# Performance work log

Measured on AMD Instinct MI355X. Metric: run time of the kernel, lower is better.

The kernel has to match this reference:

```python
import jax, jax.numpy as jnp
import numpy as np

N_NODES = 50000
D = 256
N_EDGES = 262144
N_LAYER = 3
EPS = 1e-5


def setup_inputs() -> dict:
    key = jax.random.key(0)
    ks = jax.random.split(key, 8)
    x = jax.random.normal(ks[0], (N_NODES, D), dtype=jnp.float32)
    jg_edge_index = jax.random.randint(ks[1], (2, N_EDGES), 0, N_NODES, dtype=jnp.int64)
    ln_w = jnp.ones((D,), dtype=jnp.float32)
    # torch Linear weight is [out, in]; stack per-layer weights [L, D, D]
    Ws = jax.random.normal(ks[2], (N_LAYER, D, D), dtype=jnp.float32) * (1.0 / np.sqrt(D))
    gammas = jnp.ones((N_LAYER, D), dtype=jnp.float32)
    betas = jnp.zeros((N_LAYER, D), dtype=jnp.float32)
    W_out = jax.random.normal(ks[3], (1, D), dtype=jnp.float32) * (1.0 / np.sqrt(D))
    return {"x": x, "jg_edge_index": jg_edge_index, "ln_w": ln_w,
            "Ws": Ws, "gammas": gammas, "betas": betas, "W_out": W_out}


def reference(x, jg_edge_index, ln_w, Ws, gammas, betas, W_out):
    src, dst = jg_edge_index[0], jg_edge_index[1]
    # edge features: gather + add -> [E, D]
    h = x[src, :] + x[dst, :]
    # LayerNorm over feature dim, weight only (bias=False), eps=1e-5
    mu = jnp.mean(h, axis=-1, keepdims=True)
    var = jnp.mean(jnp.square(h - mu), axis=-1, keepdims=True)
    h = (h - mu) * jax.lax.rsqrt(var + EPS) * ln_w
    # projection blocks: Linear (no bias) -> BatchNorm1d (training stats) -> ReLU
    for i in range(N_LAYER):
        h = h @ Ws[i].T  # [E, D]
        bmu = jnp.mean(h, axis=0)                      # batch mean over edges
        bvar = jnp.mean(jnp.square(h - bmu), axis=0)   # biased batch var
        h = (h - bmu) * jax.lax.rsqrt(bvar + EPS) * gammas[i] + betas[i]
        h = jax.nn.relu(h)
    logits = (h @ W_out.T).squeeze(-1)  # [E]
    return logits
```

## Files before the change

kernel.cpp:

```cpp
#include <hip/hip_runtime.h>
#include <hip/hip_bf16.h>

#define NEDGE 262144
#define DIM 256
#define NNODE 50000
#define NLAYER 3
#define EPSV 1e-5f

#define GBM 512
#define RC 64
#define NCH (GBM / RC)
#define GEMM_GRID (NEDGE / GBM)

typedef __attribute__((ext_vector_type(8))) short bf16x8_t;
typedef __attribute__((ext_vector_type(4))) float f32x4_t;

__device__ __forceinline__ float bf2f(short s) {
  unsigned u = ((unsigned)(unsigned short)s) << 16;
  return __builtin_bit_cast(float, u);
}
__device__ __forceinline__ short f2bf(float f) {
  __hip_bfloat16 h = __float2bfloat16(f);
  return __builtin_bit_cast(short, h);
}

extern "C" __global__ void __launch_bounds__(256)
k_cvt(const float* __restrict__ src, short* __restrict__ dst, int n) {
  int i = blockIdx.x * 256 + threadIdx.x;
  if (i < n) dst[i] = f2bf(src[i]);
}

extern "C" __global__ void __launch_bounds__(256)
k_cvt_x(const float* __restrict__ src, short* __restrict__ dst, int n8) {
  int i = blockIdx.x * 256 + threadIdx.x;
  if (i >= n8) return;
  const float4 a = *(const float4*)(src + (size_t)i * 8);
  const float4 b = *(const float4*)(src + (size_t)i * 8 + 4);
  bf16x8_t o;
  o[0] = f2bf(a.x); o[1] = f2bf(a.y); o[2] = f2bf(a.z); o[3] = f2bf(a.w);
  o[4] = f2bf(b.x); o[5] = f2bf(b.y); o[6] = f2bf(b.z); o[7] = f2bf(b.w);
  *(bf16x8_t*)(dst + (size_t)i * 8) = o;
}

extern "C" __global__ void __launch_bounds__(512)
k_gemm1f(const short* __restrict__ xb, const int* __restrict__ ei,
         const float* __restrict__ lnw, const short* __restrict__ W,
         short* __restrict__ C, float* __restrict__ psum, float* __restrict__ psq) {
  __shared__ short As[2][RC * DIM];
  __shared__ int sIdx[GBM], dIdx[GBM];
  const int tid = threadIdx.x;
  const int w = tid >> 6;
  const int lane = tid & 63;
  const int rl = lane & 15;
  const int kh = lane >> 4;
  const int row0 = blockIdx.x * GBM;
  const int colbase = w * 32;
  const int cst = tid & 31;

  sIdx[tid] = ei[row0 + tid];
  dIdx[tid] = ei[NEDGE + row0 + tid];

  bf16x8_t wf[2][8];
#pragma unroll
  for (int n = 0; n < 2; ++n)
#pragma unroll
    for (int ks = 0; ks < 8; ++ks)
      wf[n][ks] = *(const bf16x8_t*)(W + (size_t)(colbase + n * 16 + rl) * DIM + ks * 32 + kh * 8);

  float lw[8];
#pragma unroll
  for (int j = 0; j < 8; ++j) lw[j] = lnw[cst * 8 + j];

  float st_s0 = 0.f, st_s1 = 0.f, st_q0 = 0.f, st_q1 = 0.f;

  bf16x8_t rsA[4], rdA[4], rsB[4], rdB[4];

  auto ldgA = [&](int t) {
#pragma unroll
    for (int i = 0; i < 4; ++i) {
      const int r = (tid >> 5) + 16 * i;
      const int s = sIdx[t * RC + r];
      const int d = dIdx[t * RC + r];
      rsA[i] = *(const bf16x8_t*)(xb + (size_t)s * DIM + cst * 8);
      rdA[i] = *(const bf16x8_t*)(xb + (size_t)d * DIM + cst * 8);
    }
  };
  auto ldgB = [&](int t) {
#pragma unroll
    for (int i = 0; i < 4; ++i) {
      const int r = (tid >> 5) + 16 * i;
      const int s = sIdx[t * RC + r];
      const int d = dIdx[t * RC + r];
      rsB[i] = *(const bf16x8_t*)(xb + (size_t)s * DIM + cst * 8);
      rdB[i] = *(const bf16x8_t*)(xb + (size_t)d * DIM + cst * 8);
    }
  };

  auto lnwr = [&](int b, bf16x8_t* rs, bf16x8_t* rd) {
#pragma unroll
    for (int i = 0; i < 4; ++i) {
      const int r = (tid >> 5) + 16 * i;
      float v[8];
#pragma unroll
      for (int j = 0; j < 8; ++j) v[j] = bf2f(rs[i][j]) + bf2f(rd[i][j]);
      float s = 0.f, ss = 0.f;
#pragma unroll
      for (int j = 0; j < 8; ++j) { s += v[j]; ss = fmaf(v[j], v[j], ss); }
#pragma unroll
      for (int off = 16; off >= 1; off >>= 1) {
        s += __shfl_xor(s, off);
        ss += __shfl_xor(ss, off);
      }
      const float mu = s * (1.0f / DIM);
      const float var = ss * (1.0f / DIM) - mu * mu;
      const float sc = rsqrtf(var + EPSV);
      bf16x8_t o;
#pragma unroll
      for (int j = 0; j < 8; ++j) o[j] = f2bf((v[j] - mu) * sc * lw[j]);
      *(bf16x8_t*)(&As[b][r * DIM + ((cst ^ (r & 7)) << 3)]) = o;
    }
  };

  auto compute = [&](int t, int b) {
    const f32x4_t zero = {0.f, 0.f, 0.f, 0.f};
    f32x4_t acc[4][2];
#pragma unroll
    for (int m = 0; m < 4; ++m) { acc[m][0] = zero; acc[m][1] = zero; }
    const short* base = As[b];
#pragma unroll
    for (int ks = 0; ks < 8; ++ks) {
      bf16x8_t af[4];
#pragma unroll
      for (int m = 0; m < 4; ++m) {
        const int row = m * 16 + rl;
        const int c = ks * 4 + kh;
        af[m] = *(const bf16x8_t*)(base + row * DIM + ((c ^ (row & 7)) << 3));
      }
#pragma unroll
      for (int m = 0; m < 4; ++m) {
        acc[m][0] = __builtin_amdgcn_mfma_f32_16x16x32_bf16(af[m], wf[0][ks], acc[m][0], 0, 0, 0);
        acc[m][1] = __builtin_amdgcn_mfma_f32_16x16x32_bf16(af[m], wf[1][ks], acc[m][1], 0, 0, 0);
      }
    }
    const int rquad = kh << 2;
#pragma unroll
    for (int n = 0; n < 2; ++n) {
      const int col = colbase + n * 16 + rl;
      float s = 0.f, q = 0.f;
#pragma unroll
      for (int m = 0; m < 4; ++m) {
        const size_t rb = (size_t)(row0 + t * RC + m * 16 + rquad) * DIM + col;
#pragma unroll
        for (int r = 0; r < 4; ++r) {
          const float f = acc[m][n][r];
          C[rb + (size_t)r * DIM] = f2bf(f);
          s += f;
          q = fmaf(f, f, q);
        }
      }
      if (n == 0) { st_s0 += s; st_q0 += q; }
      else        { st_s1 += s; st_q1 += q; }
    }
  };

  __syncthreads();
  ldgA(0);
  ldgB(1);
  lnwr(0, rsA, rdA);
  __syncthreads();
  for (int t = 0; t < NCH; t += 2) {
    if (t + 2 < NCH) ldgA(t + 2);
    compute(t, 0);
    lnwr(1, rsB, rdB);
    __syncthreads();
    if (t + 3 < NCH) ldgB(t + 3);
    compute(t + 1, 1);
    if (t + 2 < NCH) lnwr(0, rsA, rdA);
    __syncthreads();
  }

  {
    float s = st_s0, q = st_q0;
    s += __shfl_xor(s, 16); s += __shfl_xor(s, 32);
    q += __shfl_xor(q, 16); q += __shfl_xor(q, 32);
    if (lane < 16) {
      psum[(size_t)blockIdx.x * DIM + colbase + rl] = s;
      psq [(size_t)blockIdx.x * DIM + colbase + rl] = q;
    }
  }
  {
    float s = st_s1, q = st_q1;
    s += __shfl_xor(s, 16); s += __shfl_xor(s, 32);
    q += __shfl_xor(q, 16); q += __shfl_xor(q, 32);
    if (lane < 16) {
      psum[(size_t)blockIdx.x * DIM + colbase + 16 + rl] = s;
      psq [(size_t)blockIdx.x * DIM + colbase + 16 + rl] = q;
    }
  }
}

extern "C" __global__ void __launch_bounds__(512, 2)
k_gemm_bn(const short* __restrict__ A, const short* __restrict__ W,
          short* __restrict__ C, float* __restrict__ psum, float* __restrict__ psq,
          const float* __restrict__ bsc, const float* __restrict__ bsh) {
  __shared__ short As[2][RC * DIM];
  const int tid = threadIdx.x;
  const int w = tid >> 6;
  const int lane = tid & 63;
  const int rl = lane & 15;
  const int kh = lane >> 4;
  const int row0 = blockIdx.x * GBM;
  const int colbase = w * 32;

  bf16x8_t wf[2][8];
#pragma unroll
  for (int n = 0; n < 2; ++n)
#pragma unroll
    for (int ks = 0; ks < 8; ++ks)
      wf[n][ks] = *(const bf16x8_t*)(W + (size_t)(colbase + n * 16 + rl) * DIM + ks * 32 + kh * 8);

  const int cst = tid & 31;
  float sc0[8], sh0[8];
#pragma unroll
  for (int j = 0; j < 8; ++j) {
    sc0[j] = bsc[cst * 8 + j];
    sh0[j] = bsh[cst * 8 + j];
  }

  float st_s0 = 0.f, st_s1 = 0.f, st_q0 = 0.f, st_q1 = 0.f;

  auto ldreg = [&](int t, bf16x8_t* r) {
#pragma unroll
    for (int i = 0; i < 4; ++i) {
      const int row = (tid + i * 512) >> 5;
      r[i] = *(const bf16x8_t*)(A + (size_t)(row0 + t * RC + row) * DIM + cst * 8);
    }
  };
  auto xform_write = [&](int b, bf16x8_t* r) {
#pragma unroll
    for (int i = 0; i < 4; ++i) {
      const int row = (tid + i * 512) >> 5;
      bf16x8_t v = r[i];
      bf16x8_t o;
#pragma unroll
      for (int j = 0; j < 8; ++j)
        o[j] = f2bf(fmaxf(fmaf(bf2f(v[j]), sc0[j], sh0[j]), 0.0f));
      *(bf16x8_t*)(&As[b][row * DIM + ((cst ^ (row & 7)) << 3)]) = o;
    }
  };

  auto compute = [&](int t, int b) {
    const f32x4_t zero = {0.f, 0.f, 0.f, 0.f};
    f32x4_t acc[4][2];
#pragma unroll
    for (int m = 0; m < 4; ++m) { acc[m][0] = zero; acc[m][1] = zero; }
    const short* base = As[b];
#pragma unroll
    for (int ks = 0; ks < 8; ++ks) {
      bf16x8_t af[4];
#pragma unroll
      for (int m = 0; m < 4; ++m) {
        const int row = m * 16 + rl;
        const int c = ks * 4 + kh;
        af[m] = *(const bf16x8_t*)(base + row * DIM + ((c ^ (row & 7)) << 3));
      }
#pragma unroll
      for (int m = 0; m < 4; ++m) {
        acc[m][0] = __builtin_amdgcn_mfma_f32_16x16x32_bf16(af[m], wf[0][ks], acc[m][0], 0, 0, 0);
        acc[m][1] = __builtin_amdgcn_mfma_f32_16x16x32_bf16(af[m], wf[1][ks], acc[m][1], 0, 0, 0);
      }
    }
    const int rquad = kh << 2;
#pragma unroll
    for (int n = 0; n < 2; ++n) {
      const int col = colbase + n * 16 + rl;
      float s = 0.f, q = 0.f;
#pragma unroll
      for (int m = 0; m < 4; ++m) {
        const size_t rb = (size_t)(row0 + t * RC + m * 16 + rquad) * DIM + col;
#pragma unroll
        for (int r = 0; r < 4; ++r) {
          const float f = acc[m][n][r];
          C[rb + (size_t)r * DIM] = f2bf(f);
          s += f;
          q = fmaf(f, f, q);
        }
      }
      if (n == 0) { st_s0 += s; st_q0 += q; }
      else        { st_s1 += s; st_q1 += q; }
    }
  };

  bf16x8_t ra[4], rb[4];
  ldreg(0, ra);
  xform_write(0, ra);
  ldreg(1, rb);
  __syncthreads();
  for (int t = 0; t < NCH; ++t) {
    if (t + 2 < NCH) ldreg(t + 2, ra);
    compute(t, t & 1);
    if (t + 1 < NCH) xform_write((t + 1) & 1, rb);
    __syncthreads();
#pragma unroll
    for (int i = 0; i < 4; ++i) { bf16x8_t tmp = ra[i]; ra[i] = rb[i]; rb[i] = tmp; }
  }

  {
    float s = st_s0, q = st_q0;
    s += __shfl_xor(s, 16); s += __shfl_xor(s, 32);
    q += __shfl_xor(q, 16); q += __shfl_xor(q, 32);
    if (lane < 16) {
      psum[(size_t)blockIdx.x * DIM + colbase + rl] = s;
      psq [(size_t)blockIdx.x * DIM + colbase + rl] = q;
    }
  }
  {
    float s = st_s1, q = st_q1;
    s += __shfl_xor(s, 16); s += __shfl_xor(s, 32);
    q += __shfl_xor(q, 16); q += __shfl_xor(q, 32);
    if (lane < 16) {
      psum[(size_t)blockIdx.x * DIM + colbase + 16 + rl] = s;
      psq [(size_t)blockIdx.x * DIM + colbase + 16 + rl] = q;
    }
  }
}

extern "C" __global__ void __launch_bounds__(64)
k_stats(const float* __restrict__ psum, const float* __restrict__ psq,
        const float* __restrict__ gamma, const float* __restrict__ beta,
        float* __restrict__ sc, float* __restrict__ sh, int nblk) {
  const int c = blockIdx.x;
  const int lane = threadIdx.x;
  float s = 0.0f, q = 0.0f;
  for (int b = lane; b < nblk; b += 64) {
    s += psum[(size_t)b * DIM + c];
    q += psq[(size_t)b * DIM + c];
  }
#pragma unroll
  for (int off = 32; off >= 1; off >>= 1) {
    s += __shfl_xor(s, off);
    q += __shfl_xor(q, off);
  }
  if (lane == 0) {
    const float inv = 1.0f / NEDGE;
    const float mu = s * inv;
    const float var = q * inv - mu * mu;
    const float scale = rsqrtf(var + EPSV) * gamma[c];
    sc[c] = scale;
    sh[c] = beta[c] - mu * scale;
  }
}

extern "C" __global__ void __launch_bounds__(256)
k_head(const short* __restrict__ h3, const float* __restrict__ sc,
       const float* __restrict__ sh, const float* __restrict__ wout,
       float* __restrict__ out) {
  const int e = (blockIdx.x << 3) + (threadIdx.x >> 5);
  const int g = threadIdx.x & 31;
  const int c = g * 8;
  const bf16x8_t v = *(const bf16x8_t*)(h3 + (size_t)e * DIM + c);
  float acc = 0.f;
#pragma unroll
  for (int j = 0; j < 8; ++j)
    acc += fmaxf(fmaf(bf2f(v[j]), sc[c + j], sh[c + j]), 0.0f) * wout[c + j];
#pragma unroll
  for (int off = 16; off >= 1; off >>= 1) acc += __shfl_xor(acc, off);
  if (g == 0) out[e] = acc;
}

extern "C" void kernel_launch(void* const* d_in, const int* in_sizes, int n_in,
                              void* d_out, int out_size, void* d_ws, size_t ws_size,
                              hipStream_t stream) {
  const float* x = (const float*)d_in[0];
  const int* ei = (const int*)d_in[1];
  const float* lnw = (const float*)d_in[2];
  const float* Ws = (const float*)d_in[3];
  const float* gammas = (const float*)d_in[4];
  const float* betas = (const float*)d_in[5];
  const float* wout = (const float*)d_in[6];
  float* out = (float*)d_out;

  char* ws = (char*)d_ws;
  const size_t HBYTES = (size_t)NEDGE * DIM * 2;
  short* h = (short*)ws;
  short* Wb = (short*)(ws + HBYTES);
  char* p = ws + HBYTES + (size_t)NLAYER * DIM * DIM * 2;
  float* psum = (float*)p;
  float* psq = psum + (size_t)GEMM_GRID * DIM;
  float* bnsc = psq + (size_t)GEMM_GRID * DIM;
  float* bnsh = bnsc + NLAYER * DIM;
  short* xb = (short*)(bnsh + NLAYER * DIM);

  k_cvt<<<(NLAYER * DIM * DIM + 255) / 256, 256, 0, stream>>>(Ws, Wb, NLAYER * DIM * DIM);
  k_cvt_x<<<(NNODE * DIM / 8 + 255) / 256, 256, 0, stream>>>(x, xb, NNODE * DIM / 8);

  k_gemm1f<<<GEMM_GRID, 512, 0, stream>>>(xb, ei, lnw, Wb, h, psum, psq);
  k_stats<<<DIM, 64, 0, stream>>>(psum, psq, gammas, betas, bnsc, bnsh, GEMM_GRID);

  for (int l = 1; l < NLAYER; ++l) {
    k_gemm_bn<<<GEMM_GRID, 512, 0, stream>>>(h, Wb + (size_t)l * DIM * DIM, h,
                                             psum, psq,
                                             bnsc + (size_t)(l - 1) * DIM,
                                             bnsh + (size_t)(l - 1) * DIM);
    k_stats<<<DIM, 64, 0, stream>>>(psum, psq, gammas + (size_t)l * DIM,
                                    betas + (size_t)l * DIM,
                                    bnsc + (size_t)l * DIM, bnsh + (size_t)l * DIM,
                                    GEMM_GRID);
  }
  k_head<<<NEDGE / 8, 256, 0, stream>>>(h, bnsc + (size_t)(NLAYER - 1) * DIM,
                                        bnsh + (size_t)(NLAYER - 1) * DIM, wout, out);
}
```

Before: 259.6 us.

## Raise GEMM-BN occupancy, stage BN scale/shift in LDS, unroll pipeline by two

The BN-fused GEMM kernel now launches with a minimum of 4 blocks per CU instead of 2. To cut register use, the per-thread BN scale/shift arrays are moved into shared memory and reloaded inside each transform. The prefetch loop is unrolled by two with fixed A/B register buffers, which removes the per-iteration register swap. The first (not-shown) GEMM kernel's C stores become nontemporal so they bypass cache retention. Risks: the tighter register budget may cause spills, and the extra LDS (two 32 KB buffers per block) may keep the occupancy target from being met.

```diff
diff --git a/kernel.cpp b/kernel.cpp
--- a/kernel.cpp
+++ b/kernel.cpp
@@ -153,7 +153,7 @@
 #pragma unroll
         for (int r = 0; r < 4; ++r) {
           const float f = acc[m][n][r];
-          C[rb + (size_t)r * DIM] = f2bf(f);
+          __builtin_nontemporal_store(f2bf(f), &C[rb + (size_t)r * DIM]);
           s += f;
           q = fmaf(f, f, q);
         }
@@ -199,11 +199,12 @@
   }
 }
 
-extern "C" __global__ void __launch_bounds__(512, 2)
+extern "C" __global__ void __launch_bounds__(512, 4)
 k_gemm_bn(const short* __restrict__ A, const short* __restrict__ W,
           short* __restrict__ C, float* __restrict__ psum, float* __restrict__ psq,
           const float* __restrict__ bsc, const float* __restrict__ bsh) {
   __shared__ short As[2][RC * DIM];
+  __shared__ float bscS[DIM], bshS[DIM];
   const int tid = threadIdx.x;
   const int w = tid >> 6;
   const int lane = tid & 63;
@@ -211,6 +212,9 @@
   const int kh = lane >> 4;
   const int row0 = blockIdx.x * GBM;
   const int colbase = w * 32;
+  const int cst = tid & 31;
+
+  if (tid < DIM) { bscS[tid] = bsc[tid]; bshS[tid] = bsh[tid]; }
 
   bf16x8_t wf[2][8];
 #pragma unroll
@@ -219,24 +223,32 @@
     for (int ks = 0; ks < 8; ++ks)
       wf[n][ks] = *(const bf16x8_t*)(W + (size_t)(colbase + n * 16 + rl) * DIM + ks * 32 + kh * 8);
 
-  const int cst = tid & 31;
-  float sc0[8], sh0[8];
-#pragma unroll
-  for (int j = 0; j < 8; ++j) {
-    sc0[j] = bsc[cst * 8 + j];
-    sh0[j] = bsh[cst * 8 + j];
-  }
-
   float st_s0 = 0.f, st_s1 = 0.f, st_q0 = 0.f, st_q1 = 0.f;
 
-  auto ldreg = [&](int t, bf16x8_t* r) {
+  bf16x8_t ra[4], rb[4];
+
+  auto ldregA = [&](int t) {
 #pragma unroll
     for (int i = 0; i < 4; ++i) {
       const int row = (tid + i * 512) >> 5;
-      r[i] = *(const bf16x8_t*)(A + (size_t)(row0 + t * RC + row) * DIM + cst * 8);
-    }
-  };
-  auto xform_write = [&](int b, bf16x8_t* r) {
+      ra[i] = *(const bf16x8_t*)(A + (size_t)(row0 + t * RC + row) * DIM + cst * 8);
+    }
+  };
+  auto ldregB = [&](int t) {
+#pragma unroll
+    for (int i = 0; i < 4; ++i) {
+      const int row = (tid + i * 512) >> 5;
+      rb[i] = *(const bf16x8_t*)(A + (size_t)(row0 + t * RC + row) * DIM + cst * 8);
+    }
+  };
+  auto xform = [&](int b, bf16x8_t* r) {
+    float cs[8], ch[8];
+    const float4 c0 = *(const float4*)&bscS[cst * 8];
+    const float4 c1 = *(const float4*)&bscS[cst * 8 + 4];
+    const float4 h0 = *(const float4*)&bshS[cst * 8];
+    const float4 h1 = *(const float4*)&bshS[cst * 8 + 4];
+    cs[0]=c0.x; cs[1]=c0.y; cs[2]=c0.z; cs[3]=c0.w; cs[4]=c1.x; cs[5]=c1.y; cs[6]=c1.z; cs[7]=c1.w;
+    ch[0]=h0.x; ch[1]=h0.y; ch[2]=h0.z; ch[3]=h0.w; ch[4]=h1.x; ch[5]=h1.y; ch[6]=h1.z; ch[7]=h1.w;
 #pragma unroll
     for (int i = 0; i < 4; ++i) {
       const int row = (tid + i * 512) >> 5;
@@ -244,7 +256,7 @@
       bf16x8_t o;
 #pragma unroll
       for (int j = 0; j < 8; ++j)
-        o[j] = f2bf(fmaxf(fmaf(bf2f(v[j]), sc0[j], sh0[j]), 0.0f));
+        o[j] = f2bf(fmaxf(fmaf(bf2f(v[j]), cs[j], ch[j]), 0.0f));
       *(bf16x8_t*)(&As[b][row * DIM + ((cst ^ (row & 7)) << 3)]) = o;
     }
   };
@@ -277,11 +289,11 @@
       float s = 0.f, q = 0.f;
 #pragma unroll
       for (int m = 0; m < 4; ++m) {
-        const size_t rb = (size_t)(row0 + t * RC + m * 16 + rquad) * DIM + col;
+        const size_t rb2 = (size_t)(row0 + t * RC + m * 16 + rquad) * DIM + col;
 #pragma unroll
         for (int r = 0; r < 4; ++r) {
           const float f = acc[m][n][r];
-          C[rb + (size_t)r * DIM] = f2bf(f);
+          C[rb2 + (size_t)r * DIM] = f2bf(f);
           s += f;
           q = fmaf(f, f, q);
         }
@@ -291,18 +303,20 @@
     }
   };
 
-  bf16x8_t ra[4], rb[4];
-  ldreg(0, ra);
-  xform_write(0, ra);
-  ldreg(1, rb);
   __syncthreads();
-  for (int t = 0; t < NCH; ++t) {
-    if (t + 2 < NCH) ldreg(t + 2, ra);
-    compute(t, t & 1);
-    if (t + 1 < NCH) xform_write((t + 1) & 1, rb);
+  ldregA(0);
+  ldregB(1);
+  xform(0, ra);
+  __syncthreads();
+  for (int t = 0; t < NCH; t += 2) {
+    if (t + 2 < NCH) ldregA(t + 2);
+    compute(t, 0);
+    xform(1, rb);
     __syncthreads();
-#pragma unroll
-    for (int i = 0; i < 4; ++i) { bf16x8_t tmp = ra[i]; ra[i] = rb[i]; rb[i] = tmp; }
+    if (t + 3 < NCH) ldregB(t + 3);
+    compute(t + 1, 1);
+    if (t + 2 < NCH) xform(0, ra);
+    __syncthreads();
   }
 
   {
```

Result: slower. 520.0 us (+100.3%).
